# Kernel optimization log

Hardware: AMD Instinct MI355X
Metric: run time of the kernel (lower is better)

## Reference

```python
import jax, jax.numpy as jnp
import numpy as np

B, N, L = 256, 128, 2048
NF, AC, HID = 75, 3, 256
DIM, NHEAD, FPD, NWORD = 128, 8, 679, 8600


def setup_inputs() -> dict:
    key = jax.random.key(0)
    ks = iter(jax.random.split(key, 48))
    rn = lambda *s: jax.random.normal(next(ks), s, dtype=jnp.float32) * 0.05
    d = {}
    d['V'] = jax.random.normal(next(ks), (B, N, NF), dtype=jnp.float32)
    d['A'] = jax.random.uniform(next(ks), (B, AC, N, N), dtype=jnp.float32)
    d['fp'] = jax.random.uniform(next(ks), (B, FPD), dtype=jnp.float32)
    d['mol_size'] = jax.random.randint(next(ks), (B,), 1, N + 1, dtype=jnp.int32)
    d['protein_seq'] = jax.random.randint(next(ks), (B, L), 0, NWORD)
    d['label'] = jax.random.randint(next(ks), (B,), 0, 2)
    # GConv blocks (multi-channel GCN): 75->256, 256->256, 256->256
    d['gc_W1'], d['gc_b1'] = rn(AC, NF, HID), rn(HID)
    d['gc_W2'], d['gc_b2'] = rn(AC, HID, HID), rn(HID)
    d['gc_W3'], d['gc_b3'] = rn(AC, HID, HID), rn(HID)
    # fp linear chain: 679->128, 128->128
    d['fp_W1'], d['fp_b1'] = rn(FPD, DIM), rn(DIM)
    d['fp_W2'], d['fp_b2'] = rn(DIM, DIM), rn(DIM)
    # global attention pooling (per-head node scores) + readout
    d['att_W'] = rn(HID, NHEAD)
    d['ro_W'], d['ro_b'] = rn(HID * NHEAD, DIM), rn(DIM)
    d['emb'] = rn(NWORD, DIM)
    # cross-attention projections
    d['mfp_W'], d['mfp_b'] = rn(DIM, DIM), rn(DIM)
    d['pfp_W'], d['pfp_b'] = rn(DIM, DIM), rn(DIM)
    d['mv_W'], d['mv_b'] = rn(DIM, DIM), rn(DIM)
    d['pv_W'], d['pv_b'] = rn(DIM, DIM), rn(DIM)
    # stacked MLPs (3 layers each, width 2*dim)
    d['mlp1_W'], d['mlp1_b'] = rn(3, 2 * DIM, 2 * DIM), rn(3, 2 * DIM)
    d['mlp2_W'], d['mlp2_b'] = rn(3, 2 * DIM, 2 * DIM), rn(3, 2 * DIM)
    d['out1_W'], d['out1_b'] = rn(2 * DIM, 2), rn(2)
    d['out2_W'], d['out2_b'] = rn(2 * DIM, 2), rn(2)
    return d


def _gconv(V, A, W, b):
    # A: [b,c,n,m], V: [b,m,f], W: [c,f,o]
    AV = jnp.einsum('bcnm,bmf->bcnf', A, V)
    return jax.nn.relu(jnp.einsum('bcnf,cfo->bno', AV, W) + b)


def _cross_attn(hvec, prot_emb, mW, mb, pW, pb):
    # hvec: [b,d]; prot_emb: [b,l,d]
    h = jax.nn.relu(hvec @ mW + mb)                       # [b,d]
    hs = jax.nn.relu(jnp.einsum('bld,de->ble', prot_emb, pW) + pb)  # [b,l,d]
    w = jnp.tanh(jnp.einsum('bd,bld->bl', h, hs))         # [b,l]
    ys = w[..., None] * hs                                 # [b,l,d]
    return jnp.max(ys, axis=1)                             # [b,d]


def reference(V, A, fp, mol_size, protein_seq, label,
              gc_W1, gc_b1, gc_W2, gc_b2, gc_W3, gc_b3,
              fp_W1, fp_b1, fp_W2, fp_b2, att_W, ro_W, ro_b, emb,
              mfp_W, mfp_b, pfp_W, pfp_b, mv_W, mv_b, pv_W, pv_b,
              mlp1_W, mlp1_b, mlp2_W, mlp2_b, out1_W, out1_b, out2_W, out2_b):
    # fp linear chain (dropout = identity at inference)
    fp = jax.nn.relu(fp @ fp_W1 + fp_b1)
    fp = jax.nn.relu(fp @ fp_W2 + fp_b2)
    # graph conv blocks
    Vh = _gconv(V, A, gc_W1, gc_b1)
    Vh = _gconv(Vh, A, gc_W2, gc_b2)
    Vh = _gconv(Vh, A, gc_W3, gc_b3)
    # masked multi-head global attention pooling over nodes
    scores = jnp.einsum('bnf,fh->bnh', Vh, att_W)          # [b,n,heads]
    mask = jnp.arange(N)[None, :] < mol_size[:, None]       # [b,n]
    scores = jnp.where(mask[..., None], scores, -1e9)
    att = jax.nn.softmax(scores, axis=1)
    pooled = jnp.einsum('bnh,bnf->bhf', att, Vh).reshape(Vh.shape[0], -1)  # [b, heads*nf]
    Vr = jax.nn.relu(pooled @ ro_W + ro_b)                  # [b,dim]
    # protein embedding + ragged cross-attention branches
    prot_emb = emb[protein_seq]                             # [b,l,dim]
    itact1 = _cross_attn(fp, prot_emb, mfp_W, mfp_b, pfp_W, pfp_b)
    itact2 = _cross_attn(Vr, prot_emb, mv_W, mv_b, pv_W, pv_b)
    cat1 = jnp.concatenate([fp, itact1], axis=1)
    cat2 = jnp.concatenate([Vr, itact2], axis=1)
    for i in range(mlp1_W.shape[0]):
        cat1 = jax.nn.relu(cat1 @ mlp1_W[i] + mlp1_b[i])
        cat2 = jax.nn.relu(cat2 @ mlp2_W[i] + mlp2_b[i])
    pred_itact = (cat1 @ out1_W + out1_b) + (cat2 @ out2_W + out2_b)
    pred_labels = jnp.argmax(pred_itact, axis=1)
    pred_scores = jax.nn.softmax(pred_itact, axis=1)[:, 1]
    return (pred_itact, label, pred_labels, pred_scores)
```

## Files before the change

### kernel.cpp

```cpp
#include <hip/hip_runtime.h>
#include <math.h>

static constexpr int BB   = 256;
static constexpr int NN   = 128;
static constexpr int LL   = 2048;
static constexpr int NF   = 75;
static constexpr int AC   = 3;
static constexpr int HID  = 256;
static constexpr int DIM  = 128;
static constexpr int NHEAD= 8;
static constexpr int FPD  = 679;
static constexpr int FPDP = 704;
static constexpr int NWORD= 8600;
static constexpr int KB   = 768;

typedef __attribute__((ext_vector_type(8))) _Float16 f16x8;
typedef __attribute__((ext_vector_type(4))) float f32x4;
typedef unsigned int u32;
typedef unsigned short u16;

__device__ __forceinline__ u16 f2h(float x) {
    _Float16 h = (_Float16)x;
    return *(u16*)&h;
}
__device__ __forceinline__ u16 f2h_sat(float x) {
    x = fminf(fmaxf(x, -65000.f), 65000.f);
    _Float16 h = (_Float16)x;
    return *(u16*)&h;
}
__device__ __forceinline__ float h2f(u16 x) {
    return (float)(*(_Float16*)&x);
}

static constexpr float AV_SCALE    = 0.0625f;
static constexpr float AV_UNSCALE  = 16.0f;

__global__ __launch_bounds__(256)
void prepA_kernel(const float* __restrict__ A, u16* __restrict__ Ah)
{
    size_t base = (size_t)blockIdx.x * (NN * NN);
    int t = threadIdx.x;
    #pragma unroll
    for (int i = 0; i < 16; ++i) {
        int id = t + i * 256;
        float4 v = *(const float4*)(A + base + (size_t)id * 4);
        u32 p0 = (u32)f2h(v.x) | ((u32)f2h(v.y) << 16);
        u32 p1 = (u32)f2h(v.z) | ((u32)f2h(v.w) << 16);
        *(uint2*)(Ah + base + (size_t)id * 4) = make_uint2(p0, p1);
    }
}

__global__ __launch_bounds__(256)
void prepFp_kernel(const float* __restrict__ fp, u16* __restrict__ fph)
{
    int b = blockIdx.x, t = threadIdx.x;
    for (int i = t; i < FPDP; i += 256) {
        float v = (i < FPD) ? fp[(size_t)b * FPD + i] : 0.f;
        fph[(size_t)b * FPDP + i] = f2h(v);
    }
}

__global__ __launch_bounds__(256)
void prepFpW_kernel(const float* __restrict__ fpW1, const float* __restrict__ fpW2,
                    u16* __restrict__ W1t, u16* __restrict__ W2t)
{
    int o = blockIdx.x, z = blockIdx.y, t = threadIdx.x;
    if (z == 0) {
        for (int k = t; k < FPDP; k += 256) {
            float v = (k < FPD) ? fpW1[(size_t)k * DIM + o] : 0.f;
            W1t[(size_t)o * FPDP + k] = f2h(v);
        }
    } else {
        if (t < 128) W2t[(size_t)o * 128 + t] = f2h(fpW2[(size_t)t * DIM + o]);
    }
}

__global__ __launch_bounds__(256)
void fp1_mfma(const u16* __restrict__ fph, const u16* __restrict__ W1t,
              const float* __restrict__ b1, u16* __restrict__ FP1h)
{
    __shared__ u16 As[128 * 40];
    __shared__ u16 Bs[128 * 40];
    int mt = blockIdx.x;
    const u16* Ap = fph + (size_t)(mt * 128) * FPDP;

    int t = threadIdx.x;
    int l = t & 63, wid = t >> 6;
    int rb = (wid >> 1) * 64, cb = (wid & 1) * 64;
    int ln = l & 15, q = l >> 4;

    f32x4 acc[4][4] = {};

    for (int kt = 0; kt < FPDP / 32; ++kt) {
        #pragma unroll
        for (int i = 0; i < 2; ++i) {
            int id = t + i * 256;
            int row = id >> 2, qh = id & 3;
            *(uint4*)&As[row * 40 + qh * 8] =
                *(const uint4*)(Ap + (size_t)row * FPDP + kt * 32 + qh * 8);
            *(uint4*)&Bs[row * 40 + qh * 8] =
                *(const uint4*)(W1t + (size_t)row * FPDP + kt * 32 + qh * 8);
        }
        __syncthreads();
        f16x8 af[4], bfr[4];
        #pragma unroll
        for (int fr = 0; fr < 4; ++fr)
            af[fr] = *(const f16x8*)&As[(rb + fr * 16 + ln) * 40 + q * 8];
        #pragma unroll
        for (int fc = 0; fc < 4; ++fc)
            bfr[fc] = *(const f16x8*)&Bs[(cb + fc * 16 + ln) * 40 + q * 8];
        #pragma unroll
        for (int fr = 0; fr < 4; ++fr)
            #pragma unroll
            for (int fc = 0; fc < 4; ++fc)
                acc[fr][fc] = __builtin_amdgcn_mfma_f32_16x16x32_f16(
                    af[fr], bfr[fc], acc[fr][fc], 0, 0, 0);
        __syncthreads();
    }
    #pragma unroll
    for (int fr = 0; fr < 4; ++fr)
        #pragma unroll
        for (int fc = 0; fc < 4; ++fc) {
            int d = cb + fc * 16 + ln;
            float bv = b1[d];
            #pragma unroll
            for (int r = 0; r < 4; ++r) {
                int m = rb + fr * 16 + q * 4 + r;
                FP1h[(size_t)(mt * 128 + m) * 128 + d] = f2h(fmaxf(acc[fr][fc][r] + bv, 0.f));
            }
        }
}

__global__ __launch_bounds__(256)
void fp2_mfma(const u16* __restrict__ FP1h, const u16* __restrict__ W2t,
              const float* __restrict__ b2, float* __restrict__ FP2)
{
    __shared__ u16 As[128 * 40];
    __shared__ u16 Bs[128 * 40];
    int mt = blockIdx.x;
    const u16* Ap = FP1h + (size_t)(mt * 128) * 128;

    int t = threadIdx.x;
    int l = t & 63, wid = t >> 6;
    int rb = (wid >> 1) * 64, cb = (wid & 1) * 64;
    int ln = l & 15, q = l >> 4;

    f32x4 acc[4][4] = {};

    for (int kt = 0; kt < 4; ++kt) {
        #pragma unroll
        for (int i = 0; i < 2; ++i) {
            int id = t + i * 256;
            int row = id >> 2, qh = id & 3;
            *(uint4*)&As[row * 40 + qh * 8] =
                *(const uint4*)(Ap + (size_t)row * 128 + kt * 32 + qh * 8);
            *(uint4*)&Bs[row * 40 + qh * 8] =
                *(const uint4*)(W2t + (size_t)row * 128 + kt * 32 + qh * 8);
        }
        __syncthreads();
        f16x8 af[4], bfr[4];
        #pragma unroll
        for (int fr = 0; fr < 4; ++fr)
            af[fr] = *(const f16x8*)&As[(rb + fr * 16 + ln) * 40 + q * 8];
        #pragma unroll
        for (int fc = 0; fc < 4; ++fc)
            bfr[fc] = *(const f16x8*)&Bs[(cb + fc * 16 + ln) * 40 + q * 8];
        #pragma unroll
        for (int fr = 0; fr < 4; ++fr)
            #pragma unroll
            for (int fc = 0; fc < 4; ++fc)
                acc[fr][fc] = __builtin_amdgcn_mfma_f32_16x16x32_f16(
                    af[fr], bfr[fc], acc[fr][fc], 0, 0, 0);
        __syncthreads();
    }
    #pragma unroll
    for (int fr = 0; fr < 4; ++fr)
        #pragma unroll
        for (int fc = 0; fc < 4; ++fc) {
            int d = cb + fc * 16 + ln;
            float bv = b2[d];
            #pragma unroll
            for (int r = 0; r < 4; ++r) {
                int m = rb + fr * 16 + q * 4 + r;
                FP2[(size_t)(mt * 128 + m) * 128 + d] = fmaxf(acc[fr][fc][r] + bv, 0.f);
            }
        }
}

__global__ __launch_bounds__(256)
void hs_kernel(const float* __restrict__ emb,
               const float* __restrict__ Wa, const float* __restrict__ ba,
               const float* __restrict__ Wb, const float* __restrict__ bb_,
               float* __restrict__ HS1, float* __restrict__ HS2)
{
    int br = blockIdx.y;
    const float* W  = br ? Wb : Wa;
    const float* bi = br ? bb_ : ba;
    float* HS = br ? HS2 : HS1;
    int half = threadIdx.x >> 7;
    int d = threadIdx.x & 127;
    int r = blockIdx.x * 2 + half;
    __shared__ float se[2][DIM];
    se[half][d] = emb[(size_t)r * DIM + d];
    __syncthreads();
    const float* er = se[half];
    float acc = 0.f;
    for (int k = 0; k < DIM; ++k) acc += er[k] * W[k * DIM + d];
    HS[(size_t)r * DIM + d] = fmaxf(acc + bi[d], 0.f);
}

__global__ __launch_bounds__(256)
void prepVt_kernel(const float* __restrict__ V, u16* __restrict__ Vt)
{
    int b = blockIdx.x, t = threadIdx.x;
    __shared__ float sV[NN * NF];
    for (int i = t; i < NN * NF; i += 256) sV[i] = V[(size_t)b * (NN * NF) + i];
    __syncthreads();
    for (int i = t; i < 80 * 128; i += 256) {
        int f = i >> 7, n = i & 127;
        float v = (f < NF) ? sV[n * NF + f] : 0.f;
        Vt[(size_t)b * (80 * 128) + i] = f2h(v);
    }
}

__global__ __launch_bounds__(256)
void prepW_kernel(const float* __restrict__ W1, const float* __restrict__ W2,
                  const float* __restrict__ W3, u16* __restrict__ Wt1,
                  u16* __restrict__ Wt2, u16* __restrict__ Wt3)
{
    int o = blockIdx.x, z = blockIdx.y, t = threadIdx.x;
    if (z == 0) {
        int k = t;
        int c = k / 80, f = k - c * 80;
        float v = (c < 3 && f < NF) ? W1[((size_t)c * NF + f) * HID + o] : 0.f;
        Wt1[(size_t)o * 256 + k] = f2h(v);
    } else {
        const float* W = (z == 1) ? W2 : W3;
        u16* Wt = (z == 1) ? Wt2 : Wt3;
        for (int k = t; k < KB; k += 256) {
            int c = k >> 8, f = k & 255;
            Wt[(size_t)o * KB + k] = f2h(W[((size_t)c * HID + f) * HID + o]);
        }
    }
}

__global__ __launch_bounds__(256)
void transp_kernel(const u16* __restrict__ H, u16* __restrict__ Ht)
{
    __shared__ u16 s[32][34];
    int o0 = blockIdx.x * 32, n0 = blockIdx.y * 32, b = blockIdx.z;
    int tx = threadIdx.x & 31, ty = threadIdx.x >> 5;
    const u16* Hp = H + (size_t)b * (NN * HID);
    #pragma unroll
    for (int j = 0; j < 4; ++j)
        s[ty + 8 * j][tx] = Hp[(size_t)(n0 + ty + 8 * j) * HID + o0 + tx];
    __syncthreads();
    u16* Hto = Ht + (size_t)b * (HID * NN);
    #pragma unroll
    for (int j = 0; j < 4; ++j)
        Hto[(size_t)(o0 + ty + 8 * j) * NN + n0 + tx] = s[tx][ty + 8 * j];
}

__global__ __launch_bounds__(256)
void gA_mfma(const u16* __restrict__ Agr, const u16* __restrict__ Htr,
             u16* __restrict__ AV, int b0, int htStride, int fpMul, int Fvalid)
{
    __shared__ u16 As[128 * 40];
    __shared__ u16 Bs[128 * 40];
    int ft = blockIdx.x, c = blockIdx.y, bl = blockIdx.z;
    int b = b0 + bl;
    const u16* Ap = Agr + ((size_t)b * AC + c) * (NN * NN);
    const u16* Bp = Htr + (size_t)b * htStride + ft * (128 * 128);
    u16* Cp = AV + (size_t)bl * (NN * KB) + c * fpMul + ft * 128;

    int t = threadIdx.x;
    int l = t & 63, wid = t >> 6;
    int rb = (wid >> 1) * 64, cb = (wid & 1) * 64;
    int ln = l & 15, q = l >> 4;

    f32x4 acc[4][4] = {};

    for (int kt = 0; kt < 4; ++kt) {
        #pragma unroll
        for (int i = 0; i < 2; ++i) {
            int id = t + i * 256;
            int row = id >> 2, qh = id & 3;
            *(uint4*)&As[row * 40 + qh * 8] =
                *(const uint4*)(Ap + (size_t)row * NN + kt * 32 + qh * 8);
        }
        #pragma unroll
        for (int i = 0; i < 2; ++i) {
            int id = t + i * 256;
            int row = id >> 2, qh = id & 3;
            uint4 v = make_uint4(0, 0, 0, 0);
            if (row < Fvalid) v = *(const uint4*)(Bp + (size_t)row * 128 + kt * 32 + qh * 8);
            *(uint4*)&Bs[row * 40 + qh * 8] = v;
        }
        __syncthreads();
        f16x8 af[4], bfr[4];
        #pragma unroll
        for (int fr = 0; fr < 4; ++fr)
            af[fr] = *(const f16x8*)&As[(rb + fr * 16 + ln) * 40 + q * 8];
        #pragma unroll
        for (int fc = 0; fc < 4; ++fc)
            bfr[fc] = *(const f16x8*)&Bs[(cb + fc * 16 + ln) * 40 + q * 8];
        #pragma unroll
        for (int fr = 0; fr < 4; ++fr)
            #pragma unroll
            for (int fc = 0; fc < 4; ++fc)
                acc[fr][fc] = __builtin_amdgcn_mfma_f32_16x16x32_f16(
                    af[fr], bfr[fc], acc[fr][fc], 0, 0, 0);
        __syncthreads();
    }
    #pragma unroll
    for (int fr = 0; fr < 4; ++fr) {
        #pragma unroll
        for (int fc = 0; fc < 4; ++fc) {
            int fcol = cb + fc * 16 + ln;
            if (fcol < Fvalid) {
                #pragma unroll
                for (int r = 0; r < 4; ++r) {
                    int n = rb + fr * 16 + q * 4 + r;
                    Cp[(size_t)n * KB + fcol] = f2h_sat(acc[fr][fc][r] * AV_SCALE);
                }
            }
        }
    }
}

__global__ __launch_bounds__(256)
void gB_mfma(const u16* __restrict__ AV, const u16* __restrict__ Wt,
             const float* __restrict__ bias, u16* __restrict__ H16,
             float* __restrict__ H32,
             int b0, int kTiles, int Ks, int outF32)
{
    __shared__ u16 As[128 * 40];
    __shared__ u16 Bs[128 * 40];
    int ot = blockIdx.x, bl = blockIdx.y;
    int b = b0 + bl;
    const u16* Ap = AV + (size_t)bl * (NN * KB);
    const u16* Bp = Wt + (size_t)ot * 128 * Ks;

    int t = threadIdx.x;
    int l = t & 63, wid = t >> 6;
    int rb = (wid >> 1) * 64, cb = (wid & 1) * 64;
    int ln = l & 15, q = l >> 4;

    f32x4 acc[4][4] = {};

    for (int kt = 0; kt < kTiles; ++kt) {
        #pragma unroll
        for (int i = 0; i < 2; ++i) {
            int id = t + i * 256;
            int row = id >> 2, qh = id & 3;
            *(uint4*)&As[row * 40 + qh * 8] =
                *(const uint4*)(Ap + (size_t)row * KB + kt * 32 + qh * 8);
            *(uint4*)&Bs[row * 40 + qh * 8] =
                *(const uint4*)(Bp + (size_t)row * Ks + kt * 32 + qh * 8);
        }
        __syncthreads();
        f16x8 af[4], bfr[4];
        #pragma unroll
        for (int fr = 0; fr < 4; ++fr)
            af[fr] = *(const f16x8*)&As[(rb + fr * 16 + ln) * 40 + q * 8];
        #pragma unroll
        for (int fc = 0; fc < 4; ++fc)
            bfr[fc] = *(const f16x8*)&Bs[(cb + fc * 16 + ln) * 40 + q * 8];
        #pragma unroll
        for (int fr = 0; fr < 4; ++fr)
            #pragma unroll
            for (int fc = 0; fc < 4; ++fc)
                acc[fr][fc] = __builtin_amdgcn_mfma_f32_16x16x32_f16(
                    af[fr], bfr[fc], acc[fr][fc], 0, 0, 0);
        __syncthreads();
    }
    #pragma unroll
    for (int fr = 0; fr < 4; ++fr) {
        #pragma unroll
        for (int fc = 0; fc < 4; ++fc) {
            int oc = cb + fc * 16 + ln;
            float bv = bias[ot * 128 + oc];
            #pragma unroll
            for (int r = 0; r < 4; ++r) {
                int n = rb + fr * 16 + q * 4 + r;
                float val = fmaxf(acc[fr][fc][r] * AV_UNSCALE + bv, 0.f);
                if (outF32)
                    H32[((size_t)b * NN + n) * HID + ot * 128 + oc] = val;
                else
                    H16[((size_t)b * NN + n) * HID + ot * 128 + oc] = f2h_sat(val);
            }
        }
    }
}

__global__ __launch_bounds__(256)
void pool_kernel(const float* __restrict__ H3,
                 const float* __restrict__ attW,
                 const int* __restrict__ msz,
                 float* __restrict__ pooled)
{
    int b = blockIdx.x, t = threadIdx.x;
    __shared__ float sW[HID * NHEAD];
    __shared__ float sS[NN * NHEAD];
    __shared__ float sT[16][264];
    __shared__ float sP[16][NHEAD][2];
    for (int i = t; i < HID * NHEAD; i += 256) sW[i] = attW[i];
    __syncthreads();
    const float* Hb = H3 + (size_t)b * NN * HID;

    for (int n0 = 0; n0 < NN; n0 += 16) {
        for (int i = t; i < 16 * 64; i += 256) {
            int row = i >> 6, fq = (i & 63) * 4;
            float4 v = *(const float4*)(Hb + (size_t)(n0 + row) * HID + fq);
            *(float4*)&sT[row][fq] = v;
        }
        __syncthreads();
        {
            int nl = t >> 4, h = (t >> 1) & 7, fh = t & 1;
            float s = 0.f;
            for (int f = fh * 128; f < fh * 128 + 128; ++f)
                s += sT[nl][f] * sW[f * NHEAD + h];
            sP[nl][h][fh] = s;
        }
        __syncthreads();
        if (t < 128) {
            int n2 = t >> 3, h2 = t & 7;
            sS[(n0 + n2) * NHEAD + h2] = sP[n2][h2][0] + sP[n2][h2][1];
        }
        __syncthreads();
    }
    int ms = msz[b];
    int h = t >> 5, ln = t & 31;
    float mx = -1e9f;
    for (int n = ln; n < NN; n += 32) {
        float s = (n < ms) ? sS[n * NHEAD + h] : -1e9f;
        mx = fmaxf(mx, s);
    }
    #pragma unroll
    for (int off = 16; off; off >>= 1) mx = fmaxf(mx, __shfl_xor(mx, off, 32));
    float sum = 0.f;
    for (int n = ln; n < NN; n += 32) {
        float s = (n < ms) ? sS[n * NHEAD + h] : -1e9f;
        sum += expf(s - mx);
    }
    #pragma unroll
    for (int off = 16; off; off >>= 1) sum += __shfl_xor(sum, off, 32);
    float inv = 1.f / sum;
    for (int n = ln; n < NN; n += 32) {
        float s = (n < ms) ? sS[n * NHEAD + h] : -1e9f;
        sS[n * NHEAD + h] = expf(s - mx) * inv;
    }
    __syncthreads();
    float accp[NHEAD] = {};
    for (int n = 0; n < NN; ++n) {
        float hv = Hb[(size_t)n * HID + t];
        #pragma unroll
        for (int hh = 0; hh < NHEAD; ++hh) accp[hh] += sS[n * NHEAD + hh] * hv;
    }
    #pragma unroll
    for (int hh = 0; hh < NHEAD; ++hh)
        pooled[(size_t)b * (HID * NHEAD) + hh * HID + t] = accp[hh];
}

__global__ __launch_bounds__(128)
void readout_part(const float* __restrict__ pooled,
                  const float* __restrict__ roW,
                  float* __restrict__ Rp)
{
    int b = blockIdx.x, s = blockIdx.y, t = threadIdx.x;
    __shared__ float sx[256];
    const float* sp = pooled + (size_t)b * (HID * NHEAD) + s * 256;
    sx[t] = sp[t];
    sx[t + 128] = sp[t + 128];
    __syncthreads();
    float acc = 0.f;
    const float* W = roW + (size_t)(s * 256) * DIM + t;
    for (int k = 0; k < 256; ++k) acc += sx[k] * W[(size_t)k * DIM];
    Rp[((size_t)s * BB + b) * DIM + t] = acc;
}

__global__ __launch_bounds__(128)
void readout_merge(const float* __restrict__ Rp,
                   const float* __restrict__ rob,
                   float* __restrict__ Vr)
{
    int b = blockIdx.x, t = threadIdx.x;
    float a = rob[t];
    #pragma unroll
    for (int s = 0; s < 8; ++s) a += Rp[((size_t)s * BB + b) * DIM + t];
    Vr[(size_t)b * DIM + t] = fmaxf(a, 0.f);
}

__global__ __launch_bounds__(128)
void atth_kernel(const float* __restrict__ FP2, const float* __restrict__ VR,
                 const float* __restrict__ mfpW, const float* __restrict__ mfpb,
                 const float* __restrict__ mvW,  const float* __restrict__ mvb,
                 float* __restrict__ h1v, float* __restrict__ h2v)
{
    int b = blockIdx.x, z = blockIdx.y, t = threadIdx.x;
    const float* in = z ? VR : FP2;
    const float* W  = z ? mvW : mfpW;
    const float* bi = z ? mvb : mfpb;
    float* out = z ? h2v : h1v;
    __shared__ float sx[DIM];
    sx[t] = in[(size_t)b * DIM + t];
    __syncthreads();
    float acc = 0.f;
    for (int k = 0; k < DIM; ++k) acc += sx[k] * W[k * DIM + t];
    out[(size_t)b * DIM + t] = fmaxf(acc + bi[t], 0.f);
}

__global__ __launch_bounds__(256)
void cross_part_kernel(const int* __restrict__ seq,
                       const float* __restrict__ HS1, const float* __restrict__ HS2,
                       const float* __restrict__ h1v, const float* __restrict__ h2v,
                       float* __restrict__ Pc)
{
    int b = blockIdx.x, s = blockIdx.y, t = threadIdx.x;
    int g = t >> 4, gl = t & 15;
    int d0 = gl * 8;
    float4 h1a = *(const float4*)(h1v + (size_t)b * DIM + d0);
    float4 h1b = *(const float4*)(h1v + (size_t)b * DIM + d0 + 4);
    float4 h2a = *(const float4*)(h2v + (size_t)b * DIM + d0);
    float4 h2b = *(const float4*)(h2v + (size_t)b * DIM + d0 + 4);
    float m1[8], m2[8];
    #pragma unroll
    for (int j = 0; j < 8; ++j) { m1[j] = -INFINITY; m2[j] = -INFINITY; }
    const int* sq = seq + (size_t)b * LL + s * 256;
    for (int it = 0; it < 16; ++it) {
        int tok = sq[g + 16 * it];
        const float4* r1 = (const float4*)(HS1 + (size_t)tok * DIM + d0);
        float4 va = r1[0], vb = r1[1];
        const float4* r2 = (const float4*)(HS2 + (size_t)tok * DIM + d0);
        float4 wa = r2[0], wb = r2[1];
        float p1 = h1a.x * va.x + h1a.y * va.y + h1a.z * va.z + h1a.w * va.w
                 + h1b.x * vb.x + h1b.y * vb.y + h1b.z * vb.z + h1b.w * vb.w;
        float p2 = h2a.x * wa.x + h2a.y * wa.y + h2a.z * wa.z + h2a.w * wa.w
                 + h2b.x * wb.x + h2b.y * wb.y + h2b.z * wb.z + h2b.w * wb.w;
        #pragma unroll
        for (int off = 8; off; off >>= 1) {
            p1 += __shfl_xor(p1, off);
            p2 += __shfl_xor(p2, off);
        }
        float w1 = tanhf(p1), w2 = tanhf(p2);
        m1[0] = fmaxf(m1[0], w1 * va.x); m1[1] = fmaxf(m1[1], w1 * va.y);
        m1[2] = fmaxf(m1[2], w1 * va.z); m1[3] = fmaxf(m1[3], w1 * va.w);
        m1[4] = fmaxf(m1[4], w1 * vb.x); m1[5] = fmaxf(m1[5], w1 * vb.y);
        m1[6] = fmaxf(m1[6], w1 * vb.z); m1[7] = fmaxf(m1[7], w1 * vb.w);
        m2[0] = fmaxf(m2[0], w2 * wa.x); m2[1] = fmaxf(m2[1], w2 * wa.y);
        m2[2] = fmaxf(m2[2], w2 * wa.z); m2[3] = fmaxf(m2[3], w2 * wa.w);
        m2[4] = fmaxf(m2[4], w2 * wb.x); m2[5] = fmaxf(m2[5], w2 * wb.y);
        m2[6] = fmaxf(m2[6], w2 * wb.z); m2[7] = fmaxf(m2[7], w2 * wb.w);
    }
    __shared__ float red[16][2][DIM];
    #pragma unroll
    for (int j = 0; j < 8; ++j) { red[g][0][d0 + j] = m1[j]; red[g][1][d0 + j] = m2[j]; }
    __syncthreads();
    int tb = t >> 7, d = t & 127;
    float mx = red[0][tb][d];
    #pragma unroll
    for (int gg = 1; gg < 16; ++gg) mx = fmaxf(mx, red[gg][tb][d]);
    Pc[(((size_t)s * BB + b) * 2 + tb) * DIM + d] = mx;
}

__global__ __launch_bounds__(256)
void cross_merge_kernel(const float* __restrict__ Pc,
                        float* __restrict__ IT1, float* __restrict__ IT2)
{
    int b = blockIdx.x, t = threadIdx.x;
    float m = -INFINITY;
    for (int s = 0; s < 8; ++s)
        m = fmaxf(m, Pc[((size_t)s * BB + b) * 256 + t]);
    if (t < DIM) IT1[(size_t)b * DIM + t] = m;
    else         IT2[(size_t)b * DIM + t - DIM] = m;
}

__global__ __launch_bounds__(512)
void mlp_kernel(const float* __restrict__ FP2, const float* __restrict__ VR,
                const float* __restrict__ IT1, const float* __restrict__ IT2,
                const float* __restrict__ m1W, const float* __restrict__ m1b,
                const float* __restrict__ m2W, const float* __restrict__ m2b,
                const float* __restrict__ o1W, const float* __restrict__ o1b,
                const float* __restrict__ o2W, const float* __restrict__ o2b,
                const int* __restrict__ label,
                float* __restrict__ dout)
{
    int b = blockIdx.x, t = threadIdx.x;
    int z = t >> 8, tt = t & 255;
    __shared__ float x[2][256], y[2][256];
    __shared__ float pl[2][256];
    {
        const float* a0 = z ? VR : FP2;
        const float* a1 = z ? IT2 : IT1;
        x[z][tt] = (tt < 128) ? a0[(size_t)b * 128 + tt] : a1[(size_t)b * 128 + tt - 128];
    }
    __syncthreads();
    for (int Lr = 0; Lr < 3; ++Lr) {
        const float* W  = (z ? m2W : m1W) + (size_t)Lr * 256 * 256;
        const float* Bv = (z ? m2b : m1b) + (size_t)Lr * 256;
        float a = 0.f;
        for (int k = 0; k < 256; ++k) a += x[z][k] * W[k * 256 + tt];
        y[z][tt] = fmaxf(a + Bv[tt], 0.f);
        __syncthreads();
        x[z][tt] = y[z][tt];
        __syncthreads();
    }
    int j = t & 1, k2 = t >> 1;
    pl[j][k2] = x[0][k2] * o1W[k2 * 2 + j] + x[1][k2] * o2W[k2 * 2 + j];
    __syncthreads();
    for (int s = 128; s > 0; s >>= 1) {
        if (k2 < s) pl[j][k2] += pl[j][k2 + s];
        __syncthreads();
    }
    if (t == 0) {
        float l0 = pl[0][0] + o1b[0] + o2b[0];
        float l1 = pl[1][0] + o1b[1] + o2b[1];
        dout[(size_t)b * 2 + 0] = l0;
        dout[(size_t)b * 2 + 1] = l1;
        dout[2 * BB + b] = (float)label[b];
        dout[3 * BB + b] = (float)((l1 > l0) ? 1 : 0);
        float mx = fmaxf(l0, l1);
        float e0 = expf(l0 - mx), e1 = expf(l1 - mx);
        dout[4 * BB + b] = e1 / (e0 + e1);
    }
}

extern "C" void kernel_launch(void* const* d_in, const int* in_sizes, int n_in,
                              void* d_out, int out_size, void* d_ws, size_t ws_size,
                              hipStream_t stream)
{
    const float* V    = (const float*)d_in[0];
    const float* A    = (const float*)d_in[1];
    const float* fp   = (const float*)d_in[2];
    const int*   msz  = (const int*)  d_in[3];
    const int*   seq  = (const int*)  d_in[4];
    const int*   lab  = (const int*)  d_in[5];
    const float* gcW1 = (const float*)d_in[6];  const float* gcb1 = (const float*)d_in[7];
    const float* gcW2 = (const float*)d_in[8];  const float* gcb2 = (const float*)d_in[9];
    const float* gcW3 = (const float*)d_in[10]; const float* gcb3 = (const float*)d_in[11];
    const float* fpW1 = (const float*)d_in[12]; const float* fpb1 = (const float*)d_in[13];
    const float* fpW2 = (const float*)d_in[14]; const float* fpb2 = (const float*)d_in[15];
    const float* attW = (const float*)d_in[16];
    const float* roW  = (const float*)d_in[17]; const float* rob  = (const float*)d_in[18];
    const float* emb  = (const float*)d_in[19];
    const float* mfpW = (const float*)d_in[20]; const float* mfpb = (const float*)d_in[21];
    const float* pfpW = (const float*)d_in[22]; const float* pfpb = (const float*)d_in[23];
    const float* mvW  = (const float*)d_in[24]; const float* mvb  = (const float*)d_in[25];
    const float* pvW  = (const float*)d_in[26]; const float* pvb  = (const float*)d_in[27];
    const float* m1W  = (const float*)d_in[28]; const float* m1b  = (const float*)d_in[29];
    const float* m2W  = (const float*)d_in[30]; const float* m2b  = (const float*)d_in[31];
    const float* o1W  = (const float*)d_in[32]; const float* o1b  = (const float*)d_in[33];
    const float* o2W  = (const float*)d_in[34]; const float* o2b  = (const float*)d_in[35];
    float* dout = (float*)d_out;

    char* ws = (char*)d_ws;
    size_t off = 0;
    auto alloc = [&](size_t bytes) -> char* {
        char* p = ws + off;
        off += (bytes + 255) & ~(size_t)255;
        return p;
    };
    u16*   Ah  = (u16*)  alloc((size_t)BB * AC * NN * NN * 2);
    u16*   Vt  = (u16*)  alloc((size_t)BB * 80 * 128 * 2);
    u16*   Wt1 = (u16*)  alloc((size_t)256 * 256 * 2);
    u16*   Wt2 = (u16*)  alloc((size_t)256 * KB * 2);
    u16*   Wt3 = (u16*)  alloc((size_t)256 * KB * 2);
    u16*   H16 = (u16*)  alloc((size_t)BB * NN * HID * 2);
    float* H3f = (float*)alloc((size_t)BB * NN * HID * 4);
    u16*   Ht  = (u16*)  alloc((size_t)BB * HID * NN * 2);
    u16*   fph = (u16*)  alloc((size_t)BB * FPDP * 2);
    u16*   W1t = (u16*)  alloc((size_t)DIM * FPDP * 2);
    u16*   W2t = (u16*)  alloc((size_t)DIM * DIM * 2);
    u16*   FP1h= (u16*)  alloc((size_t)BB * DIM * 2);
    float* FP2 = (float*)alloc((size_t)BB * DIM * 4);
    float* HS1 = (float*)alloc((size_t)NWORD * DIM * 4);
    float* HS2 = (float*)alloc((size_t)NWORD * DIM * 4);
    float* PO  = (float*)alloc((size_t)BB * HID * NHEAD * 4);
    float* VR  = (float*)alloc((size_t)BB * DIM * 4);
    float* H1V = (float*)alloc((size_t)BB * DIM * 4);
    float* H2V = (float*)alloc((size_t)BB * DIM * 4);
    float* IT1 = (float*)alloc((size_t)BB * DIM * 4);
    float* IT2 = (float*)alloc((size_t)BB * DIM * 4);
    float* Pc  = (float*)alloc((size_t)8 * BB * 2 * DIM * 4);
    float* Rp  = (float*)alloc((size_t)8 * BB * DIM * 4);
    size_t fixedBytes = off;

    int CB = 8;
    size_t perB = (size_t)NN * KB * 2;
    {
        const int tiers[] = {256, 128, 64, 32, 16, 8, 4, 2, 1};
        for (int i = 0; i < 9; ++i)
            if (fixedBytes + (size_t)tiers[i] * perB <= ws_size) { CB = tiers[i]; break; }
    }
    u16* AV = (u16*)(ws + fixedBytes);

    prepA_kernel<<<BB * AC, 256, 0, stream>>>(A, Ah);
    prepVt_kernel<<<BB, 256, 0, stream>>>(V, Vt);
    prepW_kernel<<<dim3(256, 3), 256, 0, stream>>>(gcW1, gcW2, gcW3, Wt1, Wt2, Wt3);
    prepFp_kernel<<<BB, 256, 0, stream>>>(fp, fph);
    prepFpW_kernel<<<dim3(128, 2), 256, 0, stream>>>(fpW1, fpW2, W1t, W2t);
    fp1_mfma<<<2, 256, 0, stream>>>(fph, W1t, fpb1, FP1h);
    fp2_mfma<<<2, 256, 0, stream>>>(FP1h, W2t, fpb2, FP2);
    hs_kernel<<<dim3(NWORD / 2, 2), 256, 0, stream>>>(emb, pfpW, pfpb, pvW, pvb, HS1, HS2);

    for (int b0 = 0; b0 < BB; b0 += CB) {
        gA_mfma<<<dim3(1, AC, CB), 256, 0, stream>>>(Ah, Vt, AV, b0, 80 * 128, 80, 80);
        gB_mfma<<<dim3(2, CB), 256, 0, stream>>>(AV, Wt1, gcb1, H16, H3f, b0, 8, 256, 0);
    }
    transp_kernel<<<dim3(8, 4, BB), 256, 0, stream>>>(H16, Ht);
    for (int b0 = 0; b0 < BB; b0 += CB) {
        gA_mfma<<<dim3(2, AC, CB), 256, 0, stream>>>(Ah, Ht, AV, b0, HID * NN, 256, 128);
        gB_mfma<<<dim3(2, CB), 256, 0, stream>>>(AV, Wt2, gcb2, H16, H3f, b0, 24, KB, 0);
    }
    transp_kernel<<<dim3(8, 4, BB), 256, 0, stream>>>(H16, Ht);
    for (int b0 = 0; b0 < BB; b0 += CB) {
        gA_mfma<<<dim3(2, AC, CB), 256, 0, stream>>>(Ah, Ht, AV, b0, HID * NN, 256, 128);
        gB_mfma<<<dim3(2, CB), 256, 0, stream>>>(AV, Wt3, gcb3, H16, H3f, b0, 24, KB, 1);
    }

    pool_kernel<<<BB, 256, 0, stream>>>(H3f, attW, msz, PO);
    readout_part<<<dim3(BB, 8), 128, 0, stream>>>(PO, roW, Rp);
    readout_merge<<<BB, 128, 0, stream>>>(Rp, rob, VR);
    atth_kernel<<<dim3(BB, 2), 128, 0, stream>>>(FP2, VR, mfpW, mfpb, mvW, mvb, H1V, H2V);
    cross_part_kernel<<<dim3(BB, 8), 256, 0, stream>>>(seq, HS1, HS2, H1V, H2V, Pc);
    cross_merge_kernel<<<BB, 256, 0, stream>>>(Pc, IT1, IT2);
    mlp_kernel<<<BB, 512, 0, stream>>>(FP2, VR, IT1, IT2, m1W, m1b, m2W, m2b,
                                       o1W, o1b, o2W, o2b, lab, dout);
}
```

Measured before the change: 559.4 us.

## Move protein projection, attention heads and MLP stack onto fp16 MFMA kernels

Replaces the scalar fp32 protein-embedding projection (hs_kernel), the cross-attention query projections, and the per-sample MLP stack with fp16 MFMA GEMM kernels, using pre-transposed fp16 weights. The two projected embedding tables are merged into one interleaved fp16 buffer so the gather in cross_part reads half the bytes. Intermediates are scaled to stay within fp16 range. It adds several small prep and GEMM launches and lowers precision in the tail of the network.

```diff
diff --git a/kernel.cpp b/kernel.cpp
--- a/kernel.cpp
+++ b/kernel.cpp
@@ -12,6 +12,7 @@
 static constexpr int FPD  = 679;
 static constexpr int FPDP = 704;
 static constexpr int NWORD= 8600;
+static constexpr int NWP  = 8704;
 static constexpr int KB   = 768;
 
 typedef __attribute__((ext_vector_type(8))) _Float16 f16x8;
@@ -32,8 +33,8 @@
     return (float)(*(_Float16*)&x);
 }
 
-static constexpr float AV_SCALE    = 0.0625f;
-static constexpr float AV_UNSCALE  = 16.0f;
+static constexpr float SC   = 0.0625f;
+static constexpr float USC  = 16.0f;
 
 __global__ __launch_bounds__(256)
 void prepA_kernel(const float* __restrict__ A, u16* __restrict__ Ah)
@@ -73,6 +74,27 @@
     } else {
         if (t < 128) W2t[(size_t)o * 128 + t] = f2h(fpW2[(size_t)t * DIM + o]);
     }
+}
+
+__global__ __launch_bounds__(128)
+void prepCrossW_kernel(const float* __restrict__ pfpW, const float* __restrict__ pvW,
+                       const float* __restrict__ mfpW, const float* __restrict__ mvW,
+                       u16* __restrict__ pWt12, u16* __restrict__ mWt12)
+{
+    int o = blockIdx.x, z = blockIdx.y, t = threadIdx.x;
+    const float* W = (z == 0) ? pfpW : (z == 1) ? pvW : (z == 2) ? mfpW : mvW;
+    u16* Wt = (z < 2) ? (pWt12 + (size_t)z * 128 * 128)
+                      : (mWt12 + (size_t)(z - 2) * 128 * 128);
+    Wt[(size_t)o * 128 + t] = f2h(W[(size_t)t * 128 + o]);
+}
+
+__global__ __launch_bounds__(256)
+void prepMlpW_kernel(const float* __restrict__ m1W, const float* __restrict__ m2W,
+                     u16* __restrict__ Wmlp)
+{
+    int o = blockIdx.x, Lr = blockIdx.y, br = blockIdx.z, t = threadIdx.x;
+    const float* W = (br ? m2W : m1W) + (size_t)Lr * 256 * 256;
+    Wmlp[(((size_t)(br * 3 + Lr)) * 256 + o) * 256 + t] = f2h(W[(size_t)t * 256 + o]);
 }
 
 __global__ __launch_bounds__(256)
@@ -133,7 +155,8 @@
 
 __global__ __launch_bounds__(256)
 void fp2_mfma(const u16* __restrict__ FP1h, const u16* __restrict__ W2t,
-              const float* __restrict__ b2, float* __restrict__ FP2)
+              const float* __restrict__ b2, float* __restrict__ FP2,
+              u16* __restrict__ FP2h)
 {
     __shared__ u16 As[128 * 40];
     __shared__ u16 Bs[128 * 40];
@@ -182,31 +205,82 @@
             #pragma unroll
             for (int r = 0; r < 4; ++r) {
                 int m = rb + fr * 16 + q * 4 + r;
-                FP2[(size_t)(mt * 128 + m) * 128 + d] = fmaxf(acc[fr][fc][r] + bv, 0.f);
+                float val = fmaxf(acc[fr][fc][r] + bv, 0.f);
+                FP2 [(size_t)(mt * 128 + m) * 128 + d] = val;
+                FP2h[(size_t)(mt * 128 + m) * 128 + d] = f2h(val);
             }
         }
 }
 
 __global__ __launch_bounds__(256)
-void hs_kernel(const float* __restrict__ emb,
-               const float* __restrict__ Wa, const float* __restrict__ ba,
-               const float* __restrict__ Wb, const float* __restrict__ bb_,
-               float* __restrict__ HS1, float* __restrict__ HS2)
-{
-    int br = blockIdx.y;
-    const float* W  = br ? Wb : Wa;
-    const float* bi = br ? bb_ : ba;
-    float* HS = br ? HS2 : HS1;
-    int half = threadIdx.x >> 7;
-    int d = threadIdx.x & 127;
-    int r = blockIdx.x * 2 + half;
-    __shared__ float se[2][DIM];
-    se[half][d] = emb[(size_t)r * DIM + d];
-    __syncthreads();
-    const float* er = se[half];
-    float acc = 0.f;
-    for (int k = 0; k < DIM; ++k) acc += er[k] * W[k * DIM + d];
-    HS[(size_t)r * DIM + d] = fmaxf(acc + bi[d], 0.f);
+void hs12_mfma(const float* __restrict__ emb, const u16* __restrict__ pWt12,
+               const float* __restrict__ ba, const float* __restrict__ bb_,
+               u16* __restrict__ HS12)
+{
+    __shared__ u16 As[128 * 40];
+    __shared__ u16 Bs[128 * 40];
+    int ft = blockIdx.x, br = blockIdx.y;
+    const u16* Bp = pWt12 + (size_t)br * 128 * 128;
+    const float* bias = br ? bb_ : ba;
+    int r0 = ft * 128;
+
+    int t = threadIdx.x;
+    int l = t & 63, wid = t >> 6;
+    int rb = (wid >> 1) * 64, cb = (wid & 1) * 64;
+    int ln = l & 15, q = l >> 4;
+
+    f32x4 acc[4][4] = {};
+
+    for (int kt = 0; kt < 4; ++kt) {
+        #pragma unroll
+        for (int i = 0; i < 4; ++i) {
+            int id = t + i * 256;
+            int row = id >> 3, qf = id & 7;
+            int r = r0 + row;
+            float4 v = make_float4(0.f, 0.f, 0.f, 0.f);
+            if (r < NWORD) v = *(const float4*)(emb + (size_t)r * 128 + kt * 32 + qf * 4);
+            u32 p0 = (u32)f2h(v.x) | ((u32)f2h(v.y) << 16);
+            u32 p1 = (u32)f2h(v.z) | ((u32)f2h(v.w) << 16);
+            u32* dst = (u32*)&As[row * 40 + qf * 4];
+            dst[0] = p0; dst[1] = p1;
+        }
+        #pragma unroll
+        for (int i = 0; i < 2; ++i) {
+            int id = t + i * 256;
+            int row = id >> 2, qh = id & 3;
+            *(uint4*)&Bs[row * 40 + qh * 8] =
+                *(const uint4*)(Bp + (size_t)row * 128 + kt * 32 + qh * 8);
+        }
+        __syncthreads();
+        f16x8 af[4], bfr[4];
+        #pragma unroll
+        for (int fr = 0; fr < 4; ++fr)
+            af[fr] = *(const f16x8*)&As[(rb + fr * 16 + ln) * 40 + q * 8];
+        #pragma unroll
+        for (int fc = 0; fc < 4; ++fc)
+            bfr[fc] = *(const f16x8*)&Bs[(cb + fc * 16 + ln) * 40 + q * 8];
+        #pragma unroll
+        for (int fr = 0; fr < 4; ++fr)
+            #pragma unroll
+            for (int fc = 0; fc < 4; ++fc)
+                acc[fr][fc] = __builtin_amdgcn_mfma_f32_16x16x32_f16(
+                    af[fr], bfr[fc], acc[fr][fc], 0, 0, 0);
+        __syncthreads();
+    }
+    #pragma unroll
+    for (int fr = 0; fr < 4; ++fr)
+        #pragma unroll
+        for (int fc = 0; fc < 4; ++fc) {
+            int d = cb + fc * 16 + ln;
+            float bv = bias[d];
+            #pragma unroll
+            for (int r = 0; r < 4; ++r) {
+                int m = rb + fr * 16 + q * 4 + r;
+                int rr = r0 + m;
+                if (rr < NWORD)
+                    HS12[(size_t)rr * 256 + br * 128 + d] = f2h(fmaxf(acc[fr][fc][r] + bv, 0.f));
+            }
+        }
 }
 
 __global__ __launch_bounds__(256)
@@ -321,7 +395,7 @@
                 #pragma unroll
                 for (int r = 0; r < 4; ++r) {
                     int n = rb + fr * 16 + q * 4 + r;
-                    Cp[(size_t)n * KB + fcol] = f2h_sat(acc[fr][fc][r] * AV_SCALE);
+                    Cp[(size_t)n * KB + fcol] = f2h_sat(acc[fr][fc][r] * SC);
                 }
             }
         }
@@ -383,7 +457,7 @@
             #pragma unroll
             for (int r = 0; r < 4; ++r) {
                 int n = rb + fr * 16 + q * 4 + r;
-                float val = fmaxf(acc[fr][fc][r] * AV_UNSCALE + bv, 0.f);
+                float val = fmaxf(acc[fr][fc][r] * USC + bv, 0.f);
                 if (outF32)
                     H32[((size_t)b * NN + n) * HID + ot * 128 + oc] = val;
                 else
@@ -482,75 +556,123 @@
 __global__ __launch_bounds__(128)
 void readout_merge(const float* __restrict__ Rp,
                    const float* __restrict__ rob,
-                   float* __restrict__ Vr)
+                   float* __restrict__ Vr, u16* __restrict__ Vrh)
 {
     int b = blockIdx.x, t = threadIdx.x;
     float a = rob[t];
     #pragma unroll
     for (int s = 0; s < 8; ++s) a += Rp[((size_t)s * BB + b) * DIM + t];
-    Vr[(size_t)b * DIM + t] = fmaxf(a, 0.f);
-}
-
-__global__ __launch_bounds__(128)
-void atth_kernel(const float* __restrict__ FP2, const float* __restrict__ VR,
-                 const float* __restrict__ mfpW, const float* __restrict__ mfpb,
-                 const float* __restrict__ mvW,  const float* __restrict__ mvb,
-                 float* __restrict__ h1v, float* __restrict__ h2v)
-{
-    int b = blockIdx.x, z = blockIdx.y, t = threadIdx.x;
-    const float* in = z ? VR : FP2;
-    const float* W  = z ? mvW : mfpW;
-    const float* bi = z ? mvb : mfpb;
-    float* out = z ? h2v : h1v;
-    __shared__ float sx[DIM];
-    sx[t] = in[(size_t)b * DIM + t];
-    __syncthreads();
-    float acc = 0.f;
-    for (int k = 0; k < DIM; ++k) acc += sx[k] * W[k * DIM + t];
-    out[(size_t)b * DIM + t] = fmaxf(acc + bi[t], 0.f);
+    float v = fmaxf(a, 0.f);
+    Vr [(size_t)b * DIM + t] = v;
+    Vrh[(size_t)b * DIM + t] = f2h_sat(v * SC);
+}
+
+__global__ __launch_bounds__(256)
+void atth_mfma(const u16* __restrict__ FP2h, const u16* __restrict__ VRh,
+               const u16* __restrict__ mWt12,
+               const float* __restrict__ mfpb, const float* __restrict__ mvb,
+               float* __restrict__ h1v, float* __restrict__ h2v)
+{
+    __shared__ u16 As[128 * 40];
+    __shared__ u16 Bs[128 * 40];
+    int mt = blockIdx.x, br = blockIdx.y;
+    const u16* Ap = (br ? VRh : FP2h) + (size_t)(mt * 128) * 128;
+    const u16* Bp = mWt12 + (size_t)br * 128 * 128;
+    const float* bias = br ? mvb : mfpb;
+    float unsc = br ? USC : 1.f;
+    float* out = br ? h2v : h1v;
+
+    int t = threadIdx.x;
+    int l = t & 63, wid = t >> 6;
+    int rb = (wid >> 1) * 64, cb = (wid & 1) * 64;
+    int ln = l & 15, q = l >> 4;
+
+    f32x4 acc[4][4] = {};
+
+    for (int kt = 0; kt < 4; ++kt) {
+        #pragma unroll
+        for (int i = 0; i < 2; ++i) {
+            int id = t + i * 256;
+            int row = id >> 2, qh = id & 3;
+            *(uint4*)&As[row * 40 + qh * 8] =
+                *(const uint4*)(Ap + (size_t)row * 128 + kt * 32 + qh * 8);
+            *(uint4*)&Bs[row * 40 + qh * 8] =
+                *(const uint4*)(Bp + (size_t)row * 128 + kt * 32 + qh * 8);
+        }
+        __syncthreads();
+        f16x8 af[4], bfr[4];
+        #pragma unroll
+        for (int fr = 0; fr < 4; ++fr)
+            af[fr] = *(const f16x8*)&As[(rb + fr * 16 + ln) * 40 + q * 8];
+        #pragma unroll
+        for (int fc = 0; fc < 4; ++fc)
+            bfr[fc] = *(const f16x8*)&Bs[(cb + fc * 16 + ln) * 40 + q * 8];
+        #pragma unroll
+        for (int fr = 0; fr < 4; ++fr)
+            #pragma unroll
+            for (int fc = 0; fc < 4; ++fc)
+                acc[fr][fc] = __builtin_amdgcn_mfma_f32_16x16x32_f16(
+                    af[fr], bfr[fc], acc[fr][fc], 0, 0, 0);
+        __syncthreads();
+    }
+    #pragma unroll
+    for (int fr = 0; fr < 4; ++fr)
+        #pragma unroll
+        for (int fc = 0; fc < 4; ++fc) {
+            int d = cb + fc * 16 + ln;
+            float bv = bias[d];
+            #pragma unroll
+            for (int r = 0; r < 4; ++r) {
+                int m = rb + fr * 16 + q * 4 + r;
+                out[(size_t)(mt * 128 + m) * 128 + d] = fmaxf(acc[fr][fc][r] * unsc + bv, 0.f);
+            }
+        }
 }
 
 __global__ __launch_bounds__(256)
 void cross_part_kernel(const int* __restrict__ seq,
-                       const float* __restrict__ HS1, const float* __restrict__ HS2,
+                       const u16* __restrict__ HS12,
                        const float* __restrict__ h1v, const float* __restrict__ h2v,
                        float* __restrict__ Pc)
 {
     int b = blockIdx.x, s = blockIdx.y, t = threadIdx.x;
     int g = t >> 4, gl = t & 15;
     int d0 = gl * 8;
-    float4 h1a = *(const float4*)(h1v + (size_t)b * DIM + d0);
-    float4 h1b = *(const float4*)(h1v + (size_t)b * DIM + d0 + 4);
-    float4 h2a = *(const float4*)(h2v + (size_t)b * DIM + d0);
-    float4 h2b = *(const float4*)(h2v + (size_t)b * DIM + d0 + 4);
+    float h1[8], h2[8];
+    #pragma unroll
+    for (int j = 0; j < 8; ++j) {
+        h1[j] = h1v[(size_t)b * DIM + d0 + j];
+        h2[j] = h2v[(size_t)b * DIM + d0 + j];
+    }
     float m1[8], m2[8];
     #pragma unroll
     for (int j = 0; j < 8; ++j) { m1[j] = -INFINITY; m2[j] = -INFINITY; }
     const int* sq = seq + (size_t)b * LL + s * 256;
     for (int it = 0; it < 16; ++it) {
         int tok = sq[g + 16 * it];
-        const float4* r1 = (const float4*)(HS1 + (size_t)tok * DIM + d0);
-        float4 va = r1[0], vb = r1[1];
-        const float4* r2 = (const float4*)(HS2 + (size_t)tok * DIM + d0);
-        float4 wa = r2[0], wb = r2[1];
-        float p1 = h1a.x * va.x + h1a.y * va.y + h1a.z * va.z + h1a.w * va.w
-                 + h1b.x * vb.x + h1b.y * vb.y + h1b.z * vb.z + h1b.w * vb.w;
-        float p2 = h2a.x * wa.x + h2a.y * wa.y + h2a.z * wa.z + h2a.w * wa.w
-                 + h2b.x * wb.x + h2b.y * wb.y + h2b.z * wb.z + h2b.w * wb.w;
+        const u16* r12 = HS12 + (size_t)tok * 256 + d0;
+        f16x8 va16 = *(const f16x8*)(r12);
+        f16x8 vb16 = *(const f16x8*)(r12 + 128);
+        float va[8], vb[8];
+        float p1 = 0.f, p2 = 0.f;
+        #pragma unroll
+        for (int j = 0; j < 8; ++j) {
+            va[j] = (float)va16[j];
+            vb[j] = (float)vb16[j];
+            p1 += h1[j] * va[j];
+            p2 += h2[j] * vb[j];
+        }
         #pragma unroll
         for (int off = 8; off; off >>= 1) {
             p1 += __shfl_xor(p1, off);
             p2 += __shfl_xor(p2, off);
         }
         float w1 = tanhf(p1), w2 = tanhf(p2);
-        m1[0] = fmaxf(m1[0], w1 * va.x); m1[1] = fmaxf(m1[1], w1 * va.y);
-        m1[2] = fmaxf(m1[2], w1 * va.z); m1[3] = fmaxf(m1[3], w1 * va.w);
-        m1[4] = fmaxf(m1[4], w1 * vb.x); m1[5] = fmaxf(m1[5], w1 * vb.y);
-        m1[6] = fmaxf(m1[6], w1 * vb.z); m1[7] = fmaxf(m1[7], w1 * vb.w);
-        m2[0] = fmaxf(m2[0], w2 * wa.x); m2[1] = fmaxf(m2[1], w2 * wa.y);
-        m2[2] = fmaxf(m2[2], w2 * wa.z); m2[3] = fmaxf(m2[3], w2 * wa.w);
-        m2[4] = fmaxf(m2[4], w2 * wb.x); m2[5] = fmaxf(m2[5], w2 * wb.y);
-        m2[6] = fmaxf(m2[6], w2 * wb.z); m2[7] = fmaxf(m2[7], w2 * wb.w);
+        #pragma unroll
+        for (int j = 0; j < 8; ++j) {
+            m1[j] = fmaxf(m1[j], w1 * va[j]);
+            m2[j] = fmaxf(m2[j], w2 * vb[j]);
+        }
     }
     __shared__ float red[16][2][DIM];
     #pragma unroll
@@ -575,40 +697,97 @@
     else         IT2[(size_t)b * DIM + t - DIM] = m;
 }
 
-__global__ __launch_bounds__(512)
-void mlp_kernel(const float* __restrict__ FP2, const float* __restrict__ VR,
-                const float* __restrict__ IT1, const float* __restrict__ IT2,
-                const float* __restrict__ m1W, const float* __restrict__ m1b,
-                const float* __restrict__ m2W, const float* __restrict__ m2b,
-                const float* __restrict__ o1W, const float* __restrict__ o1b,
-                const float* __restrict__ o2W, const float* __restrict__ o2b,
-                const int* __restrict__ label,
-                float* __restrict__ dout)
+__global__ __launch_bounds__(256)
+void prepX_kernel(const float* __restrict__ FP2, const float* __restrict__ VR,
+                  const float* __restrict__ IT1, const float* __restrict__ IT2,
+                  u16* __restrict__ Xh)
+{
+    int b = blockIdx.x, br = blockIdx.y, t = threadIdx.x;
+    const float* a0 = br ? VR : FP2;
+    const float* a1 = br ? IT2 : IT1;
+    float v = (t < 128) ? a0[(size_t)b * 128 + t] : a1[(size_t)b * 128 + t - 128];
+    Xh[((size_t)br * BB + b) * 256 + t] = f2h_sat(v * SC);
+}
+
+__global__ __launch_bounds__(256)
+void mlpL_mfma(const u16* __restrict__ X, const u16* __restrict__ Wmlp,
+               const float* __restrict__ m1b, const float* __restrict__ m2b,
+               int Lr, u16* __restrict__ Y)
+{
+    __shared__ u16 As[128 * 40];
+    __shared__ u16 Bs[128 * 40];
+    int mt = blockIdx.x, ot = blockIdx.y, br = blockIdx.z;
+    const u16* Ap = X + ((size_t)br * BB + mt * 128) * 256;
+    const u16* Bp = Wmlp + (((size_t)(br * 3 + Lr)) * 256 + ot * 128) * 256;
+    const float* bias = (br ? m2b : m1b) + (size_t)Lr * 256 + ot * 128;
+
+    int t = threadIdx.x;
+    int l = t & 63, wid = t >> 6;
+    int rb = (wid >> 1) * 64, cb = (wid & 1) * 64;
+    int ln = l & 15, q = l >> 4;
+
+    f32x4 acc[4][4] = {};
+
+    for (int kt = 0; kt < 8; ++kt) {
+        #pragma unroll
+        for (int i = 0; i < 2; ++i) {
+            int id = t + i * 256;
+            int row = id >> 2, qh = id & 3;
+            *(uint4*)&As[row * 40 + qh * 8] =
+                *(const uint4*)(Ap + (size_t)row * 256 + kt * 32 + qh * 8);
+            *(uint4*)&Bs[row * 40 + qh * 8] =
+                *(const uint4*)(Bp + (size_t)row * 256 + kt * 32 + qh * 8);
+        }
+        __syncthreads();
+        f16x8 af[4], bfr[4];
+        #pragma unroll
+        for (int fr = 0; fr < 4; ++fr)
+            af[fr] = *(const f16x8*)&As[(rb + fr * 16 + ln) * 40 + q * 8];
+        #pragma unroll
+        for (int fc = 0; fc < 4; ++fc)
+            bfr[fc] = *(const f16x8*)&Bs[(cb + fc * 16 + ln) * 40 + q * 8];
+        #pragma unroll
+        for (int fr = 0; fr < 4; ++fr)
+            #pragma unroll
+            for (int fc = 0; fc < 4; ++fc)
+                acc[fr][fc] = __builtin_amdgcn_mfma_f32_16x16x32_f16(
+                    af[fr], bfr[fc], acc[fr][fc], 0, 0, 0);
+        __syncthreads();
+    }
+    #pragma unroll
+    for (int fr = 0; fr < 4; ++fr)
+        #pragma unroll
+        for (int fc = 0; fc < 4; ++fc) {
+            int oc = cb + fc * 16 + ln;
+            float bv = bias[oc] * SC;
+            #pragma unroll
+            for (int r = 0; r < 4; ++r) {
+                int m = rb + fr * 16 + q * 4 + r;
+                Y[((size_t)br * BB + (mt * 128 + m)) * 256 + ot * 128 + oc] =
+                    f2h_sat(fmaxf(acc[fr][fc][r] + bv, 0.f));
+            }
+        }
+}
+
+__global__ __launch_bounds__(256)
+void mlp_out_kernel(const u16* __restrict__ Y,
+                    const float* __restrict__ o1W, const float* __restrict__ o1b,
+                    const float* __restrict__ o2W, const float* __restrict__ o2b,
+                    const int* __restrict__ label,
+                    float* __restrict__ dout)
 {
     int b = blockIdx.x, t = threadIdx.x;
-    int z = t >> 8, tt = t & 255;
-    __shared__ float x[2][256], y[2][256];
-    __shared__ float pl[2][256];
-    {
-        const float* a0 = z ? VR : FP2;
-        const float* a1 = z ? IT2 : IT1;
-        x[z][tt] = (tt < 128) ? a0[(size_t)b * 128 + tt] : a1[(size_t)b * 128 + tt - 128];
-    }
+    __shared__ float pl[2][128];
+    const u16* y1 = Y + (size_t)b * 256;
+    const u16* y2 = Y + ((size_t)BB + b) * 256;
+    int j = t & 1, k2 = t >> 1;
+    float p = USC * (h2f(y1[k2])       * o1W[k2 * 2 + j]
+                   + h2f(y1[k2 + 128]) * o1W[(k2 + 128) * 2 + j]
+                   + h2f(y2[k2])       * o2W[k2 * 2 + j]
+                   + h2f(y2[k2 + 128]) * o2W[(k2 + 128) * 2 + j]);
+    pl[j][k2] = p;
     __syncthreads();
-    for (int Lr = 0; Lr < 3; ++Lr) {
-        const float* W  = (z ? m2W : m1W) + (size_t)Lr * 256 * 256;
-        const float* Bv = (z ? m2b : m1b) + (size_t)Lr * 256;
-        float a = 0.f;
-        for (int k = 0; k < 256; ++k) a += x[z][k] * W[k * 256 + tt];
-        y[z][tt] = fmaxf(a + Bv[tt], 0.f);
-        __syncthreads();
-        x[z][tt] = y[z][tt];
-        __syncthreads();
-    }
-    int j = t & 1, k2 = t >> 1;
-    pl[j][k2] = x[0][k2] * o1W[k2 * 2 + j] + x[1][k2] * o2W[k2 * 2 + j];
-    __syncthreads();
-    for (int s = 128; s > 0; s >>= 1) {
+    for (int s = 64; s > 0; s >>= 1) {
         if (k2 < s) pl[j][k2] += pl[j][k2 + s];
         __syncthreads();
     }
@@ -660,29 +839,35 @@
         off += (bytes + 255) & ~(size_t)255;
         return p;
     };
-    u16*   Ah  = (u16*)  alloc((size_t)BB * AC * NN * NN * 2);
-    u16*   Vt  = (u16*)  alloc((size_t)BB * 80 * 128 * 2);
-    u16*   Wt1 = (u16*)  alloc((size_t)256 * 256 * 2);
-    u16*   Wt2 = (u16*)  alloc((size_t)256 * KB * 2);
-    u16*   Wt3 = (u16*)  alloc((size_t)256 * KB * 2);
-    u16*   H16 = (u16*)  alloc((size_t)BB * NN * HID * 2);
-    float* H3f = (float*)alloc((size_t)BB * NN * HID * 4);
-    u16*   Ht  = (u16*)  alloc((size_t)BB * HID * NN * 2);
-    u16*   fph = (u16*)  alloc((size_t)BB * FPDP * 2);
-    u16*   W1t = (u16*)  alloc((size_t)DIM * FPDP * 2);
-    u16*   W2t = (u16*)  alloc((size_t)DIM * DIM * 2);
-    u16*   FP1h= (u16*)  alloc((size_t)BB * DIM * 2);
-    float* FP2 = (float*)alloc((size_t)BB * DIM * 4);
-    float* HS1 = (float*)alloc((size_t)NWORD * DIM * 4);
-    float* HS2 = (float*)alloc((size_t)NWORD * DIM * 4);
-    float* PO  = (float*)alloc((size_t)BB * HID * NHEAD * 4);
-    float* VR  = (float*)alloc((size_t)BB * DIM * 4);
-    float* H1V = (float*)alloc((size_t)BB * DIM * 4);
-    float* H2V = (float*)alloc((size_t)BB * DIM * 4);
-    float* IT1 = (float*)alloc((size_t)BB * DIM * 4);
-    float* IT2 = (float*)alloc((size_t)BB * DIM * 4);
-    float* Pc  = (float*)alloc((size_t)8 * BB * 2 * DIM * 4);
-    float* Rp  = (float*)alloc((size_t)8 * BB * DIM * 4);
+    u16*   Ah    = (u16*)  alloc((size_t)BB * AC * NN * NN * 2);
+    u16*   Vt    = (u16*)  alloc((size_t)BB * 80 * 128 * 2);
+    u16*   Wt1   = (u16*)  alloc((size_t)256 * 256 * 2);
+    u16*   Wt2   = (u16*)  alloc((size_t)256 * KB * 2);
+    u16*   Wt3   = (u16*)  alloc((size_t)256 * KB * 2);
+    u16*   H16   = (u16*)  alloc((size_t)BB * NN * HID * 2);
+    float* H3f   = (float*)alloc((size_t)BB * NN * HID * 4);
+    u16*   Ht    = (u16*)  alloc((size_t)BB * HID * NN * 2);
+    u16*   fph   = (u16*)  alloc((size_t)BB * FPDP * 2);
+    u16*   W1t   = (u16*)  alloc((size_t)DIM * FPDP * 2);
+    u16*   W2t   = (u16*)  alloc((size_t)DIM * DIM * 2);
+    u16*   FP1h  = (u16*)  alloc((size_t)BB * DIM * 2);
+    float* FP2   = (float*)alloc((size_t)BB * DIM * 4);
+    u16*   FP2h  = (u16*)  alloc((size_t)BB * DIM * 2);
+    u16*   pWt12 = (u16*)  alloc((size_t)2 * 128 * 128 * 2);
+    u16*   mWt12 = (u16*)  alloc((size_t)2 * 128 * 128 * 2);
+    u16*   HS12  = (u16*)  alloc((size_t)NWP * 256 * 2);
+    float* PO    = (float*)alloc((size_t)BB * HID * NHEAD * 4);
+    float* VR    = (float*)alloc((size_t)BB * DIM * 4);
+    u16*   VRh   = (u16*)  alloc((size_t)BB * DIM * 2);
+    float* H1V   = (float*)alloc((size_t)BB * DIM * 4);
+    float* H2V   = (float*)alloc((size_t)BB * DIM * 4);
+    float* IT1   = (float*)alloc((size_t)BB * DIM * 4);
+    float* IT2   = (float*)alloc((size_t)BB * DIM * 4);
+    float* Pc    = (float*)alloc((size_t)8 * BB * 2 * DIM * 4);
+    float* Rp    = (float*)alloc((size_t)8 * BB * DIM * 4);
+    u16*   Wmlp  = (u16*)  alloc((size_t)2 * 3 * 256 * 256 * 2);
+    u16*   Xa    = (u16*)  alloc((size_t)2 * BB * 256 * 2);
+    u16*   Xb    = (u16*)  alloc((size_t)2 * BB * 256 * 2);
     size_t fixedBytes = off;
 
     int CB = 8;
@@ -699,9 +884,11 @@
     prepW_kernel<<<dim3(256, 3), 256, 0, stream>>>(gcW1, gcW2, gcW3, Wt1, Wt2, Wt3);
     prepFp_kernel<<<BB, 256, 0, stream>>>(fp, fph);
     prepFpW_kernel<<<dim3(128, 2), 256, 0, stream>>>(fpW1, fpW2, W1t, W2t);
+    prepCrossW_kernel<<<dim3(128, 4), 128, 0, stream>>>(pfpW, pvW, mfpW, mvW, pWt12, mWt12);
+    prepMlpW_kernel<<<dim3(256, 3, 2), 256, 0, stream>>>(m1W, m2W, Wmlp);
     fp1_mfma<<<2, 256, 0, stream>>>(fph, W1t, fpb1, FP1h);
-    fp2_mfma<<<2, 256, 0, stream>>>(FP1h, W2t, fpb2, FP2);
-    hs_kernel<<<dim3(NWORD / 2, 2), 256, 0, stream>>>(emb, pfpW, pfpb, pvW, pvb, HS1, HS2);
+    fp2_mfma<<<2, 256, 0, stream>>>(FP1h, W2t, fpb2, FP2, FP2h);
+    hs12_mfma<<<dim3(NWP / 128, 2), 256, 0, stream>>>(emb, pWt12, pfpb, pvb, HS12);
 
     for (int b0 = 0; b0 < BB; b0 += CB) {
         gA_mfma<<<dim3(1, AC, CB), 256, 0, stream>>>(Ah, Vt, AV, b0, 80 * 128, 80, 80);
@@ -720,10 +907,13 @@
 
     pool_kernel<<<BB, 256, 0, stream>>>(H3f, attW, msz, PO);
     readout_part<<<dim3(BB, 8), 128, 0, stream>>>(PO, roW, Rp);
-    readout_merge<<<BB, 128, 0, stream>>>(Rp, rob, VR);
-    atth_kernel<<<dim3(BB, 2), 128, 0, stream>>>(FP2, VR, mfpW, mfpb, mvW, mvb, H1V, H2V);
-    cross_part_kernel<<<dim3(BB, 8), 256, 0, stream>>>(seq, HS1, HS2, H1V, H2V, Pc);
+    readout_merge<<<BB, 128, 0, stream>>>(Rp, rob, VR, VRh);
+    atth_mfma<<<dim3(2, 2), 256, 0, stream>>>(FP2h, VRh, mWt12, mfpb, mvb, H1V, H2V);
+    cross_part_kernel<<<dim3(BB, 8), 256, 0, stream>>>(seq, HS12, H1V, H2V, Pc);
     cross_merge_kernel<<<BB, 256, 0, stream>>>(Pc, IT1, IT2);
-    mlp_kernel<<<BB, 512, 0, stream>>>(FP2, VR, IT1, IT2, m1W, m1b, m2W, m2b,
-                                       o1W, o1b, o2W, o2b, lab, dout);
-}
+    prepX_kernel<<<dim3(BB, 2), 256, 0, stream>>>(FP2, VR, IT1, IT2, Xa);
+    mlpL_mfma<<<dim3(2, 2, 2), 256, 0, stream>>>(Xa, Wmlp, m1b, m2b, 0, Xb);
+    mlpL_mfma<<<dim3(2, 2, 2), 256, 0, stream>>>(Xb, Wmlp, m1b, m2b, 1, Xa);
+    mlpL_mfma<<<dim3(2, 2, 2), 256, 0, stream>>>(Xa, Wmlp, m1b, m2b, 2, Xb);
+    mlp_out_kernel<<<BB, 256, 0, stream>>>(Xb, o1W, o1b, o2W, o2b, lab, dout);
+}
```

Result: faster. 535.9 us (-4.2%).
